# Optimization experiments

Measured on AMD Instinct MI355X. Metric: run time of the kernel, lower is better.

The kernel has to match this reference:

```python
import jax, jax.numpy as jnp
import numpy as np

# Static configuration matching init_kwargs / layer defaults
NX, NY, NZ = 512, 512, 32
BATCH = 32
STEP_V = [3, 1, 3]
STEP_H = [1, 5]
FRAC_V = [1/3, 1/3, 1/3]
FRAC_H = [1/4, 3/4]
K1 = np.array([[1., 2., 1.], [2., 4., 2.], [1., 2., 1.]], dtype=np.float32)


def _sample_indices(n, steps, fracs, scale_n):
    """Replicates the while-loop stride schedule in MyLayer.call.

    Appends the current index, THEN checks whether it crossed the
    cumulative-fraction boundary (cumsum(frac[:s+1]) * scale_n - 1),
    bumping the stride index when it does. scale_n mirrors the original
    code's (swapped) use of the opposite spatial dim; with a square
    image it equals n.
    """
    cf = np.cumsum(fracs)
    idxs, cur, s = [], 0, 0
    while cur < n - 2:
        idxs.append(cur)
        if s < len(cf) and cur > cf[s] * scale_n - 1:
            s += 1
        cur += steps[min(s, len(steps) - 1)]
    return np.array(idxs, dtype=np.int32)

ROWS = _sample_indices(NX, STEP_V, FRAC_V, NY)  # row (vertical) sample starts
COLS = _sample_indices(NY, STEP_H, FRAC_H, NX)  # col (horizontal) sample starts


def setup_inputs() -> dict:
    key = jax.random.key(0)
    x = jax.random.normal(key, (BATCH, NX, NY, NZ), dtype=jnp.float32)
    return {"x": x}


def reference(x):
    # out[b, i, j, c] = sum_{di,dj} K1[di,dj] * x[b, ROWS[i]+di, COLS[j]+dj, c]
    # 9 static gathers + fused weighted sum; kernel broadcast over channels
    # (kernel is repeated per-channel in the original, i.e. depthwise).
    k = jnp.asarray(K1, dtype=x.dtype)
    out = jnp.zeros((x.shape[0], ROWS.shape[0], COLS.shape[0], x.shape[3]), dtype=x.dtype)
    for di in range(3):
        xi = x[:, ROWS + di]            # [B, out_v, NY, C]
        for dj in range(3):
            out = out + k[di, dj] * xi[:, :, COLS + dj]  # [B, out_v, out_h, C]
    return out
```

## Files before the change

### kernel.cpp

```cpp
#include <hip/hip_runtime.h>


#define B_   32
#define NX_  512
#define NY_  512
#define NZ_  32
#define NR_  284
#define NC_  205
#define ZQ_  (NZ_/4)

__device__ __forceinline__ int row_of(int r) {
    return (r < 58) ? 3 * r : ((r < 228) ? r + 114 : 3 * r - 340);
}
__device__ __forceinline__ int col_of(int c) {
    return (c < 129) ? c : 5 * c - 512;
}

__global__ __launch_bounds__(256)
void blur_sample_kernel(const float* __restrict__ x, float* __restrict__ out) {
    const int zq = threadIdx.x & 7;
    const int cl = threadIdx.x >> 3;
    const int c  = blockIdx.x * 32 + cl;
    const int r  = blockIdx.y;
    const int b  = blockIdx.z;
    if (c >= NC_) return;

    const int row0 = row_of(r);
    const int col0 = col_of(c);

    const float4* xp = reinterpret_cast<const float4*>(x)
                     + ((size_t)(b * NX_ + row0) * NY_ + col0) * ZQ_ + zq;

    float4 acc = make_float4(0.f, 0.f, 0.f, 0.f);
    #pragma unroll
    for (int di = 0; di < 3; ++di) {
        const float4* p = xp + (size_t)di * (NY_ * ZQ_);
        const float4 a  = p[0];
        const float4 bb = p[ZQ_];
        const float4 cc = p[2 * ZQ_];
        const float w = (di == 1) ? 2.0f : 1.0f;
        acc.x += w * (a.x + 2.0f * bb.x + cc.x);
        acc.y += w * (a.y + 2.0f * bb.y + cc.y);
        acc.z += w * (a.z + 2.0f * bb.z + cc.z);
        acc.w += w * (a.w + 2.0f * bb.w + cc.w);
    }

    float4* op = reinterpret_cast<float4*>(out)
               + ((size_t)(b * NR_ + r) * NC_ + c) * ZQ_ + zq;
    *op = acc;
}

extern "C" void kernel_launch(void* const* d_in, const int* in_sizes, int n_in,
                              void* d_out, int out_size, void* d_ws, size_t ws_size,
                              hipStream_t stream) {
    const float* x = (const float*)d_in[0];
    float* out = (float*)d_out;
    dim3 block(256);
    dim3 grid((NC_ + 31) / 32, NR_, B_);
    blur_sample_kernel<<<grid, block, 0, stream>>>(x, out);
}
```

Before: 208.3 us.

## Process 8 output rows per thread with rolling horizontal-sum register reuse

Each thread now computes eight consecutive output rows instead of one. It keeps the three horizontal partial sums in registers and, where the row schedule advances by one (the middle stride-1 region), loads only one new input row per output. This cuts redundant global and cache loads of overlapping rows. The cost is fewer blocks and a serial loop per thread, which lowers parallelism and may reduce latency hiding, while the stride-3 regions gain little.

```diff
diff --git a/kernel.cpp b/kernel.cpp
--- a/kernel.cpp
+++ b/kernel.cpp
@@ -8,6 +8,7 @@
 #define NR_  284
 #define NC_  205
 #define ZQ_  (NZ_/4)
+#define R_   8
 
 __device__ __forceinline__ int row_of(int r) {
     return (r < 58) ? 3 * r : ((r < 228) ? r + 114 : 3 * r - 340);
@@ -17,37 +18,62 @@
 }
 
 __global__ __launch_bounds__(256)
-void blur_sample_kernel(const float* __restrict__ x, float* __restrict__ out) {
+void blur_roll_kernel(const float* __restrict__ x, float* __restrict__ out) {
     const int zq = threadIdx.x & 7;
     const int cl = threadIdx.x >> 3;
     const int c  = blockIdx.x * 32 + cl;
-    const int r  = blockIdx.y;
+    const int r0 = blockIdx.y * R_;
     const int b  = blockIdx.z;
     if (c >= NC_) return;
 
-    const int row0 = row_of(r);
     const int col0 = col_of(c);
+    const float4* xb = reinterpret_cast<const float4*>(x)
+                     + (size_t)b * (NX_ * NY_ * ZQ_) + zq;
+    float4* ob = reinterpret_cast<float4*>(out)
+               + ((size_t)b * NR_ * NC_) * ZQ_ + (size_t)c * ZQ_ + zq;
 
-    const float4* xp = reinterpret_cast<const float4*>(x)
-                     + ((size_t)(b * NX_ + row0) * NY_ + col0) * ZQ_ + zq;
-
-    float4 acc = make_float4(0.f, 0.f, 0.f, 0.f);
-    #pragma unroll
-    for (int di = 0; di < 3; ++di) {
-        const float4* p = xp + (size_t)di * (NY_ * ZQ_);
+    auto hsum = [&](int row) -> float4 {
+        const float4* p = xb + ((size_t)row * NY_ + col0) * ZQ_;
         const float4 a  = p[0];
         const float4 bb = p[ZQ_];
         const float4 cc = p[2 * ZQ_];
-        const float w = (di == 1) ? 2.0f : 1.0f;
-        acc.x += w * (a.x + 2.0f * bb.x + cc.x);
-        acc.y += w * (a.y + 2.0f * bb.y + cc.y);
-        acc.z += w * (a.z + 2.0f * bb.z + cc.z);
-        acc.w += w * (a.w + 2.0f * bb.w + cc.w);
+        float4 h;
+        h.x = (a.x + cc.x) + 2.0f * bb.x;
+        h.y = (a.y + cc.y) + 2.0f * bb.y;
+        h.z = (a.z + cc.z) + 2.0f * bb.z;
+        h.w = (a.w + cc.w) + 2.0f * bb.w;
+        return h;
+    };
+    auto vsum = [](const float4& h0, const float4& h1, const float4& h2) -> float4 {
+        float4 v;
+        v.x = (h0.x + h2.x) + 2.0f * h1.x;
+        v.y = (h0.y + h2.y) + 2.0f * h1.y;
+        v.z = (h0.z + h2.z) + 2.0f * h1.z;
+        v.w = (h0.w + h2.w) + 2.0f * h1.w;
+        return v;
+    };
+
+    const int rEnd = (r0 + R_ < NR_) ? r0 + R_ : NR_;
+
+    int row = row_of(r0);
+    float4 h0 = hsum(row);
+    float4 h1 = hsum(row + 1);
+    float4 h2 = hsum(row + 2);
+    ob[(size_t)r0 * NC_ * ZQ_] = vsum(h0, h1, h2);
+
+    for (int rr = r0 + 1; rr < rEnd; ++rr) {
+        const int nrow = row_of(rr);
+        if (nrow == row + 1) {
+            h0 = h1; h1 = h2;
+            h2 = hsum(nrow + 2);
+        } else {
+            h0 = hsum(nrow);
+            h1 = hsum(nrow + 1);
+            h2 = hsum(nrow + 2);
+        }
+        row = nrow;
+        ob[(size_t)rr * NC_ * ZQ_] = vsum(h0, h1, h2);
     }
-
-    float4* op = reinterpret_cast<float4*>(out)
-               + ((size_t)(b * NR_ + r) * NC_ + c) * ZQ_ + zq;
-    *op = acc;
 }
 
 extern "C" void kernel_launch(void* const* d_in, const int* in_sizes, int n_in,
@@ -56,6 +82,6 @@
     const float* x = (const float*)d_in[0];
     float* out = (float*)d_out;
     dim3 block(256);
-    dim3 grid((NC_ + 31) / 32, NR_, B_);
-    blur_sample_kernel<<<grid, block, 0, stream>>>(x, out);
+    dim3 grid((NC_ + 31) / 32, (NR_ + R_ - 1) / R_, B_);
+    blur_roll_kernel<<<grid, block, 0, stream>>>(x, out);
 }
```

New measurement: 205.5 us. About the same (-1.4%).
